# Performance work log

Hardware: AMD Instinct MI355X
Metric: run time of the kernel (lower is better)

The kernel has to match this reference:

```python
import jax, jax.numpy as jnp
import numpy as np

NEG = -1e30  # safe 'log zero' for fp32 (avoids -inf NaNs in grads)


def _ctc_loss(logits, targets, input_lengths, target_lengths):
    """PyTorch-semantics CTC loss: blank=0, reduction='mean', zero_infinity=True.
    logits: [B,T,C] (pre-log-softmax), targets: [B,S] padded, lengths: [B].
    """
    B, T, C = logits.shape
    S = targets.shape[1]
    L = 2 * S + 1  # extended target length (blanks interleaved)
    logp = jax.nn.log_softmax(logits, axis=-1)  # [B,T,C]

    # extended targets: blank, y1, blank, y2, ..., blank
    ext = jnp.zeros((B, L), jnp.int32).at[:, 1::2].set(targets.astype(jnp.int32))
    lp_ext = jnp.take_along_axis(
        logp, jnp.broadcast_to(ext[:, None, :], (B, T, L)), axis=2)  # [B,T,L]

    pos = jnp.arange(L)
    ext_m2 = jnp.pad(ext, ((0, 0), (2, 0)))[:, :L]
    can_skip = (ext != 0) & (ext != ext_m2) & (pos >= 2)  # [B,L]

    def shift(a, k):
        return jnp.pad(a, ((0, 0), (k, 0)), constant_values=NEG)[:, :L]

    def lse3(a, b, c):
        m = jnp.maximum(jnp.maximum(a, b), c)
        return m + jnp.log(jnp.exp(a - m) + jnp.exp(b - m) + jnp.exp(c - m))

    alpha0 = (jnp.full((B, L), NEG, logits.dtype)
              .at[:, 0].set(lp_ext[:, 0, 0])
              .at[:, 1].set(lp_ext[:, 0, 1]))

    def step(alpha, xs):
        lp_t, t = xs  # lp_t: [B,L]
        a2 = shift(alpha, 1)
        a3 = jnp.where(can_skip, shift(alpha, 2), NEG)
        new = lp_t + lse3(alpha, a2, a3)
        # freeze alpha once past each sample's input_length
        alpha = jnp.where((t < input_lengths)[:, None], new, alpha)
        return alpha, None

    lp_T = jnp.swapaxes(lp_ext, 0, 1)  # [T,B,L]
    alpha, _ = jax.lax.scan(step, alpha0, (lp_T[1:], jnp.arange(1, T)))

    i1 = (2 * target_lengths - 1).astype(jnp.int32)
    i2 = (2 * target_lengths).astype(jnp.int32)
    a_last = jnp.take_along_axis(alpha, i1[:, None], axis=1)[:, 0]
    a_blank = jnp.take_along_axis(alpha, i2[:, None], axis=1)[:, 0]
    loss = -jnp.logaddexp(a_last, a_blank)  # [B]
    loss = jnp.where(loss > 1e29, 0.0, loss)  # zero_infinity=True
    return jnp.mean(loss / target_lengths.astype(loss.dtype))


def setup_inputs() -> dict:
    key = jax.random.key(0)
    ks = jax.random.split(key, 8)
    B, T = 32, 2000
    C_err, S_err = 4, 50
    C_ph, S_ph = 64, 200
    error_logits = jax.random.normal(ks[0], (B, T, C_err), jnp.float32)
    phoneme_logits = jax.random.normal(ks[1], (B, T, C_ph), jnp.float32)
    # labels in [1, C): blank=0 never appears in targets
    error_targets = jax.random.randint(ks[2], (B, S_err), 1, C_err, jnp.int32)
    phoneme_targets = jax.random.randint(ks[3], (B, S_ph), 1, C_ph, jnp.int32)
    error_input_lengths = jax.random.randint(ks[4], (B,), T - T // 4, T + 1, jnp.int32)
    phoneme_input_lengths = jax.random.randint(ks[5], (B,), T - T // 4, T + 1, jnp.int32)
    error_target_lengths = jax.random.randint(ks[6], (B,), S_err // 2, S_err + 1, jnp.int32)
    phoneme_target_lengths = jax.random.randint(ks[7], (B,), S_ph // 2, S_ph + 1, jnp.int32)
    return {
        "error_logits": error_logits,
        "phoneme_logits": phoneme_logits,
        "error_targets": error_targets,
        "phoneme_targets": phoneme_targets,
        "error_input_lengths": error_input_lengths,
        "phoneme_input_lengths": phoneme_input_lengths,
        "error_target_lengths": error_target_lengths,
        "phoneme_target_lengths": phoneme_target_lengths,
    }


def reference(error_logits, phoneme_logits, error_targets, phoneme_targets,
              error_input_lengths, phoneme_input_lengths,
              error_target_lengths, phoneme_target_lengths):
    error_weight = 1.0
    phoneme_weight = 1.0
    error_loss = _ctc_loss(error_logits, error_targets,
                           error_input_lengths, error_target_lengths)
    phoneme_loss = _ctc_loss(phoneme_logits, phoneme_targets,
                             phoneme_input_lengths, phoneme_target_lengths)
    total_loss = error_weight * error_loss + phoneme_weight * phoneme_loss
    return total_loss
```

## Files before the change

kernel.cpp:

```cpp
#include <hip/hip_runtime.h>
#include <math.h>


static constexpr float  LOG2E = 1.4426950408889634f;
static constexpr double LN2D  = 0.6931471805599453;
static constexpr int GROWS = 2032;

#define DPP_WAVE_SHL1   0x130
#define DPP_WAVE_SHR1   0x138
#define DPP_ROW_SHR(n)  (0x110 | (n))
#define DPP_ROW_BCAST15 0x142
#define DPP_ROW_BCAST31 0x143

__device__ __forceinline__ float fexp2(float x) {
  return __builtin_amdgcn_exp2f(x);
}
__device__ __forceinline__ float flog2(float x) {
  return __builtin_amdgcn_logf(x);
}

__device__ __forceinline__ double dpp_shr1_f64(double x) {
  int lo = __double2loint(x), hi = __double2hiint(x);
  lo = __builtin_amdgcn_update_dpp(0, lo, DPP_WAVE_SHR1, 0xf, 0xf, true);
  hi = __builtin_amdgcn_update_dpp(0, hi, DPP_WAVE_SHR1, 0xf, 0xf, true);
  return __hiloint2double(hi, lo);
}

__device__ __forceinline__ double dpp_shl1_f64(double x) {
  int lo = __double2loint(x), hi = __double2hiint(x);
  lo = __builtin_amdgcn_update_dpp(0, lo, DPP_WAVE_SHL1, 0xf, 0xf, true);
  hi = __builtin_amdgcn_update_dpp(0, hi, DPP_WAVE_SHL1, 0xf, 0xf, true);
  return __hiloint2double(hi, lo);
}

__device__ __forceinline__ int imax2(int a, int b) { return a > b ? a : b; }

__device__ __forceinline__ int wave_imax(int v) {
  v = imax2(v, __builtin_amdgcn_update_dpp(0, v, DPP_ROW_SHR(1), 0xf, 0xf, true));
  v = imax2(v, __builtin_amdgcn_update_dpp(0, v, DPP_ROW_SHR(2), 0xf, 0xf, true));
  v = imax2(v, __builtin_amdgcn_update_dpp(0, v, DPP_ROW_SHR(4), 0xf, 0xf, true));
  v = imax2(v, __builtin_amdgcn_update_dpp(0, v, DPP_ROW_SHR(8), 0xf, 0xf, true));
  v = imax2(v, __builtin_amdgcn_update_dpp(0, v, DPP_ROW_BCAST15, 0xf, 0xf, true));
  v = imax2(v, __builtin_amdgcn_update_dpp(0, v, DPP_ROW_BCAST31, 0xf, 0xf, true));
  return __builtin_amdgcn_readlane(v, 63);
}


__global__ __launch_bounds__(256) void gather_ph_kernel(
    const float* __restrict__ ph_logits, const float* __restrict__ err_logits,
    const int* __restrict__ ph_tgt,
    float* __restrict__ Gph, float* __restrict__ Lpb_ph,
    float* __restrict__ Lpb_er, float* __restrict__ out) {
  const int bx = blockIdx.x, b = blockIdx.y;
  const int tid = threadIdx.x;
  const int lane = tid & 63, wv = tid >> 6;

  if (bx == 0 && b == 0 && tid == 0) *out = 0.f;

  if (wv == 0 && lane < 32) {
    const int t = bx * 32 + lane;
    if (t < 2000) {
      const float4 v = *(const float4*)(err_logits + ((size_t)b * 2000 + t) * 4);
      const float z0 = v.x * LOG2E;
      const float s = fexp2(z0) + fexp2(v.y * LOG2E) + fexp2(v.z * LOG2E) +
                      fexp2(v.w * LOG2E);
      Lpb_er[(size_t)b * GROWS + t] = z0 - flog2(s);
    }
  }

  const int* tb = ph_tgt + b * 200;
  int idx[4];
  float msk[4];
#pragma unroll
  for (int k = 0; k < 4; ++k) {
    const int si = lane * 4 + k;
    const int cls = (si < 200) ? tb[si] : 0;
    idx[k] = cls << 2;
    msk[k] = (si < 200) ? 1.0f : 0.0f;
  }
  const int t0 = (bx * 4 + wv) * 8;
  float z[8], e[8], s[8];
#pragma unroll
  for (int u = 0; u < 8; ++u) {
    const int t = t0 + u;
    const int tc = (t < 2000) ? t : 1999;
    z[u] = ph_logits[((size_t)b * 2000 + tc) * 64 + lane] * LOG2E;
    e[u] = fexp2(z[u]);
    s[u] = e[u];
  }
#pragma unroll
  for (int off = 32; off >= 1; off >>= 1) {
#pragma unroll
    for (int u = 0; u < 8; ++u) s[u] += __shfl_xor(s[u], off, 64);
  }
#pragma unroll
  for (int u = 0; u < 8; ++u) {
    const int t = t0 + u;
    if (t < 2000) {
      const float e0 = __int_as_float(
          __builtin_amdgcn_readlane(__float_as_int(e[u]), 0));
      const float inv0 = 1.0f / e0;
      float o[4];
#pragma unroll
      for (int k = 0; k < 4; ++k) {
        const float v = __int_as_float(
            __builtin_amdgcn_ds_bpermute(idx[k], __float_as_int(e[u])));
        o[k] = msk[k] * v * inv0;
      }
      *(float4*)(Gph + ((size_t)b * GROWS + t) * 256 + lane * 4) =
          make_float4(o[0], o[1], o[2], o[3]);
      if (lane == 0)
        Lpb_ph[(size_t)b * GROWS + t] = z[u] - flog2(s[u]);
    }
  }
}

template <int P> struct RowP { float v[P]; };

template <int P>
__device__ __forceinline__ void bl_renorm(double (&B)[P], double (&L)[P],
                                          int& K, int tgt) {
  double mm = B[0];
#pragma unroll
  for (int k = 0; k < P; ++k) mm = fmax(fmax(mm, B[k]), L[k]);
  const int ex = (__double2hiint(mm) >> 20) & 0x7ff;
  const int emax = wave_imax(ex);
  if (emax > 0) {
    int d = tgt - emax;
    if (d > 1023) d = 1023;
    if (d < -1022) d = -1022;
    const double sc = __hiloint2double((d + 1023) << 20, 0);
#pragma unroll
    for (int k = 0; k < P; ++k) { B[k] *= sc; L[k] *= sc; }
    K += d;
  }
}

template <int P>
__device__ __forceinline__ void bl_step(double (&B)[P], double (&L)[P],
                                        const double (&skipm)[P],
                                        const RowP<P>& f) {
  const double Lm1 = dpp_shr1_f64(L[P - 1]);
  double nB[P], nL[P];
#pragma unroll
  for (int k = 0; k < P; ++k) {
    const double Lp = (k >= 1) ? L[k - 1] : Lm1;
    nB[k] = B[k] + Lp;
    nL[k] = (double)f.v[k] * fma(skipm[k], Lp, B[k] + L[k]);
  }
#pragma unroll
  for (int k = 0; k < P; ++k) { B[k] = nB[k]; L[k] = nL[k]; }
}

template <int P>
__device__ __forceinline__ void bl_step_bwd(double (&B)[P], double (&L)[P],
                                            const double (&sknext)[P],
                                            const RowP<P>& f) {
  double w[P];
#pragma unroll
  for (int k = 0; k < P; ++k) w[k] = (double)f.v[k] * L[k];
  const double wN = dpp_shl1_f64(w[0]);
  const double BN = dpp_shl1_f64(B[0]);
  double nB[P], nL[P];
#pragma unroll
  for (int k = 0; k < P; ++k) {
    const double wp1 = (k < P - 1) ? w[k + 1] : wN;
    const double Bp1 = (k < P - 1) ? B[k + 1] : BN;
    nB[k] = B[k] + w[k];
    nL[k] = fma(sknext[k], wp1, w[k] + Bp1);
  }
#pragma unroll
  for (int k = 0; k < P; ++k) { B[k] = nB[k]; L[k] = nL[k]; }
}

__device__ __forceinline__ float spb_sum(const float* __restrict__ Lpb,
                                         int len, int lane) {
  float spb = 0.f;
  for (int t0 = lane; t0 < len; t0 += 512) {
#pragma unroll
    for (int u = 0; u < 8; ++u) {
      const int t = t0 + u * 64;
      const int tc = (t < len) ? t : 0;
      const float v = Lpb[tc];
      spb += (t < len) ? v : 0.0f;
    }
  }
#pragma unroll
  for (int off = 32; off >= 1; off >>= 1) spb += __shfl_xor(spb, off, 64);
  return spb;
}

template <int P, typename LdF, typename UseF>
__device__ __forceinline__ void run_fwd(int nsteps, LdF ldrow, UseF use,
                                        double (&B)[P], double (&L)[P],
                                        const double (&sk)[P], int& K) {
  using Buf = decltype(ldrow(1));
  const int ng = nsteps / 16;
  Buf bufA[16], bufB[16];
  if (ng >= 1) {
#pragma unroll
    for (int u = 0; u < 16; ++u) bufA[u] = ldrow(1 + u);
  }
  if (ng >= 2) {
#pragma unroll
    for (int u = 0; u < 16; ++u) bufB[u] = ldrow(17 + u);
  }
  int g = 0;
  for (; g + 2 <= ng; g += 2) {
    bl_renorm<P>(B, L, K, 1523);
    {
      const int gn = (g + 2 < ng) ? (g + 2) : 0;
#pragma unroll
      for (int u = 0; u < 16; ++u) {
        bl_step<P>(B, L, sk, use(bufA[u]));
        bufA[u] = ldrow(1 + gn * 16 + u);
      }
    }
    bl_renorm<P>(B, L, K, 1523);
    {
      const int gn = (g + 3 < ng) ? (g + 3) : 0;
#pragma unroll
      for (int u = 0; u < 16; ++u) {
        bl_step<P>(B, L, sk, use(bufB[u]));
        bufB[u] = ldrow(1 + gn * 16 + u);
      }
    }
  }
  if (g < ng) {
    bl_renorm<P>(B, L, K, 1523);
#pragma unroll
    for (int u = 0; u < 16; ++u) bl_step<P>(B, L, sk, use(bufA[u]));
    ++g;
  }
  {
    const int tstart = 1 + ng * 16;
    Buf bufT[15];
#pragma unroll
    for (int u = 0; u < 15; ++u) {
      int t = tstart + u;
      if (t > nsteps) t = (nsteps > 0) ? nsteps : 1;
      bufT[u] = ldrow(t);
    }
#pragma unroll
    for (int u = 0; u < 15; ++u) {
      if (tstart + u <= nsteps) {
        if (u == 0) bl_renorm<P>(B, L, K, 1523);
        bl_step<P>(B, L, sk, use(bufT[u]));
      }
    }
  }
}

template <int P, typename LdF, typename UseF>
__device__ __forceinline__ void run_bwd(int len, int M, LdF ldrow, UseF use,
                                        double (&B)[P], double (&L)[P],
                                        const double (&sk)[P], int& K) {
  using Buf = decltype(ldrow(1));
  const int ng = M / 16;
  Buf bufA[16], bufB[16];
  if (ng >= 1) {
#pragma unroll
    for (int u = 0; u < 16; ++u) bufA[u] = ldrow(len - 1 - u);
  }
  if (ng >= 2) {
#pragma unroll
    for (int u = 0; u < 16; ++u) bufB[u] = ldrow(len - 17 - u);
  }
  int g = 0;
  for (; g + 2 <= ng; g += 2) {
    bl_renorm<P>(B, L, K, 1023);
    {
      const int jb = (g + 2 < ng) ? (g + 2) * 16 : 0;
#pragma unroll
      for (int u = 0; u < 16; ++u) {
        bl_step_bwd<P>(B, L, sk, use(bufA[u]));
        bufA[u] = ldrow(len - 1 - jb - u);
      }
    }
    bl_renorm<P>(B, L, K, 1023);
    {
      const int jb = (g + 3 < ng) ? (g + 3) * 16 : 0;
#pragma unroll
      for (int u = 0; u < 16; ++u) {
        bl_step_bwd<P>(B, L, sk, use(bufB[u]));
        bufB[u] = ldrow(len - 1 - jb - u);
      }
    }
  }
  if (g < ng) {
    bl_renorm<P>(B, L, K, 1023);
#pragma unroll
    for (int u = 0; u < 16; ++u) bl_step_bwd<P>(B, L, sk, use(bufA[u]));
    ++g;
  }
  {
    const int jstart = ng * 16;
    Buf bufT[15];
#pragma unroll
    for (int u = 0; u < 15; ++u) {
      int j = jstart + u;
      if (j > M - 1) j = (M > 0) ? (M - 1) : 0;
      bufT[u] = ldrow(len - 1 - j);
    }
#pragma unroll
    for (int u = 0; u < 15; ++u) {
      if (jstart + u < M) {
        if (u == 0) bl_renorm<P>(B, L, K, 1023);
        bl_step_bwd<P>(B, L, sk, use(bufT[u]));
      }
    }
  }
}

__device__ __forceinline__ void chain_ph_fb(
    const float* __restrict__ Glab, const float* __restrict__ Lpb,
    const int* __restrict__ tb, int len, int tl, float* __restrict__ out,
    double* sBb, double* sLb, int* sKb) {
  constexpr int P = 4, S = 200, LSTRIDE = 256;
  const int tid = threadIdx.x;
  const int wave = tid >> 6, lane = tid & 63;
  const int t_mid = len >> 1;
  const int M = (len - 1) - t_mid;
  const float* gp = Glab + lane * P;

  auto ldrow = [&](int t) {
    RowP<P> r;
    const float4 a = *(const float4*)(gp + (size_t)t * LSTRIDE);
    r.v[0] = a.x; r.v[1] = a.y; r.v[2] = a.z; r.v[3] = a.w;
    return r;
  };
  auto use_id = [](const RowP<P>& r) { return r; };

  float spb = 0.f;
  double B[P], L[P];
  int Kf = 0;

  if (wave == 0) {
    spb = spb_sum(Lpb, len, lane);
    double skipm[P];
#pragma unroll
    for (int k = 0; k < P; ++k) {
      const int s = lane * P + k;
      skipm[k] = (s >= 1 && s < S && tb[s] != tb[s - 1]) ? 1.0 : 0.0;
    }
#pragma unroll
    for (int k = 0; k < P; ++k) { B[k] = 0.0; L[k] = 0.0; }
    {
      const float r0 = Glab[0];
      if (lane == 0) { B[0] = 1.0; L[0] = (double)r0; }
    }
    run_fwd<P>(t_mid, ldrow, use_id, B, L, skipm, Kf);
  } else {
    double sknext[P];
#pragma unroll
    for (int k = 0; k < P; ++k) {
      const int s = lane * P + k;
      sknext[k] = (s + 1 < S && tb[s + 1] != tb[s]) ? 1.0 : 0.0;
    }
    double Bb[P], Lb[P];
#pragma unroll
    for (int k = 0; k < P; ++k) {
      const int s = lane * P + k;
      Bb[k] = (s == tl) ? 1.0 : 0.0;
      Lb[k] = (s == tl - 1) ? 1.0 : 0.0;
    }
    int Kb = 0;
    run_bwd<P>(len, M, ldrow, use_id, Bb, Lb, sknext, Kb);
#pragma unroll
    for (int k = 0; k < P; ++k) {
      sBb[lane * P + k] = Bb[k];
      sLb[lane * P + k] = Lb[k];
    }
    if (lane == 0) *sKb = Kb;
  }
  __syncthreads();
  if (wave == 0) {
    double dot = 0.0;
#pragma unroll
    for (int k = 0; k < P; ++k)
      dot += B[k] * sBb[lane * P + k] + L[k] * sLb[lane * P + k];
#pragma unroll
    for (int off = 32; off >= 1; off >>= 1) dot += __shfl_xor(dot, off, 64);
    if (lane == 0) {
      const int K2 = Kf + *sKb;
      float loss = (float)((double)K2 * LN2D - log(dot) - (double)spb * LN2D);
      if (!(loss < 1e29f)) loss = 0.f;
      atomicAdd(out, loss / ((float)tl * 32.0f));
    }
  }
}

__device__ __forceinline__ void chain_er_fb(
    const float* __restrict__ zb, const float* __restrict__ Lpb,
    const int* __restrict__ tb, int len, int tl, float* __restrict__ out,
    double* sBb, double* sLb, int* sKb) {
  constexpr int P = 1, S = 50;
  const int tid = threadIdx.x;
  const int wave = tid >> 6, lane = tid & 63;
  const int t_mid = len >> 1;
  const int M = (len - 1) - t_mid;
  const float4* zr = (const float4*)zb;

  const int c1 = tb[(lane < S) ? lane : (S - 1)];
  const float fmask = (lane < S) ? 1.0f : 0.0f;

  auto ldrow = [&](int t) { return zr[t]; };
  auto mkf = [&](const float4& q) {
    RowP<P> f;
    const float zc = (c1 == 1) ? q.y : (c1 == 2) ? q.z : q.w;
    f.v[0] = fmask * fexp2((zc - q.x) * LOG2E);
    return f;
  };

  float spb = 0.f;
  double B[P], L[P];
  int Kf = 0;

  if (wave == 0) {
    spb = spb_sum(Lpb, len, lane);
    double skipm[P];
    skipm[0] =
        (lane >= 1 && lane < S && tb[lane] != tb[lane - 1]) ? 1.0 : 0.0;
    B[0] = 0.0; L[0] = 0.0;
    {
      const float4 q0 = zr[0];
      const int c0 = tb[0];
      const float zc = (c0 == 1) ? q0.y : (c0 == 2) ? q0.z : q0.w;
      if (lane == 0) {
        B[0] = 1.0;
        L[0] = (double)fexp2((zc - q0.x) * LOG2E);
      }
    }
    run_fwd<P>(t_mid, ldrow, mkf, B, L, skipm, Kf);
  } else {
    double sknext[P];
    sknext[0] = (lane + 1 < S && tb[lane + 1] != tb[lane]) ? 1.0 : 0.0;
    double Bb[P], Lb[P];
    Bb[0] = (lane == tl) ? 1.0 : 0.0;
    Lb[0] = (lane == tl - 1) ? 1.0 : 0.0;
    int Kb = 0;
    run_bwd<P>(len, M, ldrow, mkf, Bb, Lb, sknext, Kb);
    sBb[lane] = Bb[0];
    sLb[lane] = Lb[0];
    if (lane == 0) *sKb = Kb;
  }
  __syncthreads();
  if (wave == 0) {
    double dot = B[0] * sBb[lane] + L[0] * sLb[lane];
#pragma unroll
    for (int off = 32; off >= 1; off >>= 1) dot += __shfl_xor(dot, off, 64);
    if (lane == 0) {
      const int K2 = Kf + *sKb;
      float loss = (float)((double)K2 * LN2D - log(dot) - (double)spb * LN2D);
      if (!(loss < 1e29f)) loss = 0.f;
      atomicAdd(out, loss / ((float)tl * 32.0f));
    }
  }
}

__global__ __launch_bounds__(128) void ctc_chains_fbsplit_kernel(
    const float* __restrict__ Gph, const float* __restrict__ err_logits,
    const int* __restrict__ ph_tgt, const int* __restrict__ err_tgt,
    const int* __restrict__ err_il, const int* __restrict__ ph_il,
    const int* __restrict__ err_tl, const int* __restrict__ ph_tl,
    const float* __restrict__ Lpb_ph, const float* __restrict__ Lpb_er,
    float* __restrict__ out) {
  __shared__ double sBb[256], sLb[256];
  __shared__ int sKb;
  const int blk = blockIdx.x;
  if (blk < 32) {
    int len = err_il[blk]; if (len > 2000) len = 2000;
    chain_er_fb(err_logits + (size_t)blk * 2000 * 4,
                Lpb_er + (size_t)blk * GROWS, err_tgt + blk * 50, len,
                err_tl[blk], out, sBb, sLb, &sKb);
  } else {
    const int b = blk - 32;
    int len = ph_il[b]; if (len > 2000) len = 2000;
    chain_ph_fb(Gph + (size_t)b * GROWS * 256,
                Lpb_ph + (size_t)b * GROWS, ph_tgt + b * 200, len,
                ph_tl[b], out, sBb, sLb, &sKb);
  }
}


__global__ __launch_bounds__(256) void softmax4_kernel(
    const float* __restrict__ x, float* __restrict__ p, int nrows) {
  int r = blockIdx.x * blockDim.x + threadIdx.x;
  if (r >= nrows) return;
  float4 v = *reinterpret_cast<const float4*>(x + (size_t)r * 4);
  float z0 = v.x * LOG2E, z1 = v.y * LOG2E, z2 = v.z * LOG2E, z3 = v.w * LOG2E;
  float m = fmaxf(fmaxf(z0, z1), fmaxf(z2, z3));
  float e0 = fexp2(z0 - m), e1 = fexp2(z1 - m);
  float e2 = fexp2(z2 - m), e3 = fexp2(z3 - m);
  float inv = 1.0f / (e0 + e1 + e2 + e3);
  float4 o;
  o.x = e0 * inv; o.y = e1 * inv; o.z = e2 * inv; o.w = e3 * inv;
  *reinterpret_cast<float4*>(p + (size_t)r * 4) = o;
}

__global__ __launch_bounds__(256) void softmax64_kernel(
    const float* __restrict__ x, float* __restrict__ p, int nrows) {
  int row = blockIdx.x * 4 + (threadIdx.x >> 6);
  int lane = threadIdx.x & 63;
  if (row >= nrows) return;
  float z = x[(size_t)row * 64 + lane] * LOG2E;
  float m = z;
#pragma unroll
  for (int off = 32; off >= 1; off >>= 1) m = fmaxf(m, __shfl_xor(m, off, 64));
  float e = fexp2(z - m);
  float s = e;
#pragma unroll
  for (int off = 32; off >= 1; off >>= 1) s += __shfl_xor(s, off, 64);
  p[(size_t)row * 64 + lane] = e * (1.0f / s);
}

template <int C, int S, int R>
__device__ __forceinline__ void ctc_chain_lin_fb(
    const float* __restrict__ p_b, const int* __restrict__ tgt_b,
    int len, int tl, float* __restrict__ out, double* sa) {
  constexpr int L = 2 * S + 1;
  const int lane = threadIdx.x;
  int idx[R];
  double skipm[R];
#pragma unroll
  for (int j = 0; j < R; ++j) {
    const int l = lane * R + j;
    int cls = 0;
    bool sk = false;
    if (l & 1) {
      const int s = (l - 1) >> 1;
      const int sc = (s < S) ? s : (S - 1);
      cls = tgt_b[sc];
      if (s >= 1 && s < S) sk = (cls != tgt_b[s - 1]);
    }
    idx[j] = cls * 4;
    skipm[j] = sk ? 1.0 : 0.0;
  }
  double alpha[R];
#pragma unroll
  for (int j = 0; j < R; ++j) {
    const int l = lane * R + j;
    alpha[j] = (l <= 1) ? (double)p_b[idx[j] >> 2] : 0.0;
  }
  int K = 0;
  const int cl = lane & (C - 1);
  float rv = p_b[(size_t)((1 < len - 1) ? 1 : (len - 1)) * C + cl];
  float pf[R];
#pragma unroll
  for (int j = 0; j < R; ++j)
    pf[j] = __int_as_float(__builtin_amdgcn_ds_bpermute(idx[j], __float_as_int(rv)));
  rv = p_b[(size_t)((2 < len - 1) ? 2 : (len - 1)) * C + cl];
  for (int t = 1; t < len; ++t) {
    if ((t & 31) == 0) {
      double m = alpha[0];
#pragma unroll
      for (int j = 1; j < R; ++j) m = fmax(m, alpha[j]);
#pragma unroll
      for (int off = 1; off < 64; off <<= 1) m = fmax(m, __shfl_xor(m, off, 64));
      const long long bits = __double_as_longlong(m);
      const int e = (int)((bits >> 52) & 0x7FF);
      if (e > 0) {
        const double sc = __longlong_as_double((long long)(2046 - e) << 52);
#pragma unroll
        for (int j = 0; j < R; ++j) alpha[j] *= sc;
        K += 1023 - e;
      }
    }
    const int tn = (t + 2 < len) ? (t + 2) : (len - 1);
    const float rvn = p_b[(size_t)tn * C + cl];
    float pfn[R];
#pragma unroll
    for (int j = 0; j < R; ++j)
      pfn[j] = __int_as_float(__builtin_amdgcn_ds_bpermute(idx[j], __float_as_int(rv)));
    double am1 = __shfl_up(alpha[R - 1], 1, 64);
    double am2 = __shfl_up(alpha[R - 2], 1, 64);
    if (lane == 0) { am1 = 0.0; am2 = 0.0; }
    double na[R];
#pragma unroll
    for (int j = 0; j < R; ++j) {
      const double a0 = alpha[j];
      const double a1 = (j >= 1) ? alpha[j - 1] : am1;
      const double a2 = (j >= 2) ? alpha[j - 2] : ((j == 1) ? am1 : am2);
      double s = a0 + a1;
      s = fma(skipm[j], a2, s);
      na[j] = (double)pf[j] * s;
    }
#pragma unroll
    for (int j = 0; j < R; ++j) alpha[j] = na[j];
#pragma unroll
    for (int j = 0; j < R; ++j) pf[j] = pfn[j];
    rv = rvn;
  }
#pragma unroll
  for (int j = 0; j < R; ++j) {
    const int l = lane * R + j;
    if (l < L) sa[l] = alpha[j];
  }
  __syncthreads();
  if (lane == 0) {
    const double a = sa[2 * tl - 1] + sa[2 * tl];
    float loss = (float)((double)K * LN2D - log(a));
    if (!(loss < 1e29f)) loss = 0.0f;
    atomicAdd(out, loss / ((float)tl * 32.0f));
  }
}

__global__ __launch_bounds__(64) void ctc_chains_fb_kernel(
    const float* __restrict__ p_err, const float* __restrict__ p_ph,
    const int* __restrict__ err_tgt, const int* __restrict__ ph_tgt,
    const int* __restrict__ err_il, const int* __restrict__ ph_il,
    const int* __restrict__ err_tl, const int* __restrict__ ph_tl,
    float* __restrict__ out) {
  __shared__ double sa[512];
  const int T = 2000;
  const int blk = blockIdx.x;
  if (blk < 32) {
    const int b = blk;
    int len = err_il[b]; if (len > T) len = T;
    ctc_chain_lin_fb<4, 50, 2>(p_err + (size_t)b * T * 4, err_tgt + b * 50, len,
                               err_tl[b], out, sa);
  } else {
    const int b = blk - 32;
    int len = ph_il[b]; if (len > T) len = T;
    ctc_chain_lin_fb<64, 200, 7>(p_ph + (size_t)b * T * 64, ph_tgt + b * 200,
                                 len, ph_tl[b], out, sa);
  }
}


extern "C" void kernel_launch(void* const* d_in, const int* in_sizes, int n_in,
                              void* d_out, int out_size, void* d_ws,
                              size_t ws_size, hipStream_t stream) {
  const float* err_logits = (const float*)d_in[0];
  const float* ph_logits  = (const float*)d_in[1];
  const int* err_tgt = (const int*)d_in[2];
  const int* ph_tgt  = (const int*)d_in[3];
  const int* err_il  = (const int*)d_in[4];
  const int* ph_il   = (const int*)d_in[5];
  const int* err_tl  = (const int*)d_in[6];
  const int* ph_tl   = (const int*)d_in[7];
  float* out = (float*)d_out;

  const size_t gph = (size_t)32 * GROWS * 256;
  const size_t lpb = (size_t)32 * GROWS;
  const size_t need = (gph + 2 * lpb) * sizeof(float);

  if (ws_size >= need) {
    float* Gph = (float*)d_ws;
    float* Lpb_ph = Gph + gph;
    float* Lpb_er = Lpb_ph + lpb;
    gather_ph_kernel<<<dim3(63, 32), 256, 0, stream>>>(
        ph_logits, err_logits, ph_tgt, Gph, Lpb_ph, Lpb_er, out);
    ctc_chains_fbsplit_kernel<<<64, 128, 0, stream>>>(
        Gph, err_logits, ph_tgt, err_tgt, err_il, ph_il, err_tl, ph_tl,
        Lpb_ph, Lpb_er, out);
  } else {
    (void)hipMemsetAsync(d_out, 0, sizeof(float), stream);
    const int B = 32, T = 2000;
    const int rows = B * T;
    float* p_err = (float*)d_ws;
    float* p_ph  = p_err + (size_t)rows * 4;
    softmax4_kernel<<<(rows + 255) / 256, 256, 0, stream>>>(err_logits, p_err, rows);
    softmax64_kernel<<<(rows + 3) / 4, 256, 0, stream>>>(ph_logits, p_ph, rows);
    ctc_chains_fb_kernel<<<64, 64, 0, stream>>>(p_err, p_ph, err_tgt, ph_tgt,
                                                err_il, ph_il, err_tl, ph_tl, out);
  }
}
```

Baseline: 204.2 us.

## Split forward and backward CTC halves into separate one-wave blocks with merge kernel

Instead of a 128-thread block per chain with wave 0 running the forward half and wave 1 the backward half, each direction now runs in its own 64-thread block (128 blocks total). The two halves write their states to global workspace, and a new merge kernel computes the dot product and loss. This spreads the two serial recurrences across separate CUs instead of sharing one CU's SIMD resources. In exchange it adds a kernel launch and a global-memory round trip for the intermediate states.

Result: no change. 202.2 us (-1.0%).

```diff
diff --git a/kernel.cpp b/kernel.cpp
--- a/kernel.cpp
+++ b/kernel.cpp
@@ -312,173 +312,161 @@
   }
 }
 
-__device__ __forceinline__ void chain_ph_fb(
-    const float* __restrict__ Glab, const float* __restrict__ Lpb,
-    const int* __restrict__ tb, int len, int tl, float* __restrict__ out,
-    double* sBb, double* sLb, int* sKb) {
-  constexpr int P = 4, S = 200, LSTRIDE = 256;
-  const int tid = threadIdx.x;
-  const int wave = tid >> 6, lane = tid & 63;
-  const int t_mid = len >> 1;
-  const int M = (len - 1) - t_mid;
-  const float* gp = Glab + lane * P;
-
-  auto ldrow = [&](int t) {
-    RowP<P> r;
-    const float4 a = *(const float4*)(gp + (size_t)t * LSTRIDE);
-    r.v[0] = a.x; r.v[1] = a.y; r.v[2] = a.z; r.v[3] = a.w;
-    return r;
-  };
-  auto use_id = [](const RowP<P>& r) { return r; };
-
-  float spb = 0.f;
-  double B[P], L[P];
-  int Kf = 0;
-
-  if (wave == 0) {
-    spb = spb_sum(Lpb, len, lane);
-    double skipm[P];
-#pragma unroll
-    for (int k = 0; k < P; ++k) {
-      const int s = lane * P + k;
-      skipm[k] = (s >= 1 && s < S && tb[s] != tb[s - 1]) ? 1.0 : 0.0;
-    }
-#pragma unroll
-    for (int k = 0; k < P; ++k) { B[k] = 0.0; L[k] = 0.0; }
-    {
-      const float r0 = Glab[0];
-      if (lane == 0) { B[0] = 1.0; L[0] = (double)r0; }
-    }
-    run_fwd<P>(t_mid, ldrow, use_id, B, L, skipm, Kf);
-  } else {
-    double sknext[P];
-#pragma unroll
-    for (int k = 0; k < P; ++k) {
-      const int s = lane * P + k;
-      sknext[k] = (s + 1 < S && tb[s + 1] != tb[s]) ? 1.0 : 0.0;
-    }
-    double Bb[P], Lb[P];
-#pragma unroll
-    for (int k = 0; k < P; ++k) {
-      const int s = lane * P + k;
-      Bb[k] = (s == tl) ? 1.0 : 0.0;
-      Lb[k] = (s == tl - 1) ? 1.0 : 0.0;
-    }
-    int Kb = 0;
-    run_bwd<P>(len, M, ldrow, use_id, Bb, Lb, sknext, Kb);
-#pragma unroll
-    for (int k = 0; k < P; ++k) {
-      sBb[lane * P + k] = Bb[k];
-      sLb[lane * P + k] = Lb[k];
-    }
-    if (lane == 0) *sKb = Kb;
-  }
-  __syncthreads();
-  if (wave == 0) {
-    double dot = 0.0;
-#pragma unroll
-    for (int k = 0; k < P; ++k)
-      dot += B[k] * sBb[lane * P + k] + L[k] * sLb[lane * P + k];
-#pragma unroll
-    for (int off = 32; off >= 1; off >>= 1) dot += __shfl_xor(dot, off, 64);
-    if (lane == 0) {
-      const int K2 = Kf + *sKb;
-      float loss = (float)((double)K2 * LN2D - log(dot) - (double)spb * LN2D);
-      if (!(loss < 1e29f)) loss = 0.f;
-      atomicAdd(out, loss / ((float)tl * 32.0f));
-    }
-  }
-}
-
-__device__ __forceinline__ void chain_er_fb(
-    const float* __restrict__ zb, const float* __restrict__ Lpb,
-    const int* __restrict__ tb, int len, int tl, float* __restrict__ out,
-    double* sBb, double* sLb, int* sKb) {
-  constexpr int P = 1, S = 50;
-  const int tid = threadIdx.x;
-  const int wave = tid >> 6, lane = tid & 63;
-  const int t_mid = len >> 1;
-  const int M = (len - 1) - t_mid;
-  const float4* zr = (const float4*)zb;
-
-  const int c1 = tb[(lane < S) ? lane : (S - 1)];
-  const float fmask = (lane < S) ? 1.0f : 0.0f;
-
-  auto ldrow = [&](int t) { return zr[t]; };
-  auto mkf = [&](const float4& q) {
-    RowP<P> f;
-    const float zc = (c1 == 1) ? q.y : (c1 == 2) ? q.z : q.w;
-    f.v[0] = fmask * fexp2((zc - q.x) * LOG2E);
-    return f;
-  };
-
-  float spb = 0.f;
-  double B[P], L[P];
-  int Kf = 0;
-
-  if (wave == 0) {
-    spb = spb_sum(Lpb, len, lane);
-    double skipm[P];
-    skipm[0] =
-        (lane >= 1 && lane < S && tb[lane] != tb[lane - 1]) ? 1.0 : 0.0;
-    B[0] = 0.0; L[0] = 0.0;
-    {
-      const float4 q0 = zr[0];
-      const int c0 = tb[0];
-      const float zc = (c0 == 1) ? q0.y : (c0 == 2) ? q0.z : q0.w;
-      if (lane == 0) {
-        B[0] = 1.0;
-        L[0] = (double)fexp2((zc - q0.x) * LOG2E);
-      }
-    }
-    run_fwd<P>(t_mid, ldrow, mkf, B, L, skipm, Kf);
-  } else {
-    double sknext[P];
-    sknext[0] = (lane + 1 < S && tb[lane + 1] != tb[lane]) ? 1.0 : 0.0;
-    double Bb[P], Lb[P];
-    Bb[0] = (lane == tl) ? 1.0 : 0.0;
-    Lb[0] = (lane == tl - 1) ? 1.0 : 0.0;
-    int Kb = 0;
-    run_bwd<P>(len, M, ldrow, mkf, Bb, Lb, sknext, Kb);
-    sBb[lane] = Bb[0];
-    sLb[lane] = Lb[0];
-    if (lane == 0) *sKb = Kb;
-  }
-  __syncthreads();
-  if (wave == 0) {
-    double dot = B[0] * sBb[lane] + L[0] * sLb[lane];
-#pragma unroll
-    for (int off = 32; off >= 1; off >>= 1) dot += __shfl_xor(dot, off, 64);
-    if (lane == 0) {
-      const int K2 = Kf + *sKb;
-      float loss = (float)((double)K2 * LN2D - log(dot) - (double)spb * LN2D);
-      if (!(loss < 1e29f)) loss = 0.f;
-      atomicAdd(out, loss / ((float)tl * 32.0f));
-    }
-  }
-}
-
-__global__ __launch_bounds__(128) void ctc_chains_fbsplit_kernel(
+__global__ __launch_bounds__(64) void ctc_half_kernel(
     const float* __restrict__ Gph, const float* __restrict__ err_logits,
     const int* __restrict__ ph_tgt, const int* __restrict__ err_tgt,
     const int* __restrict__ err_il, const int* __restrict__ ph_il,
     const int* __restrict__ err_tl, const int* __restrict__ ph_tl,
     const float* __restrict__ Lpb_ph, const float* __restrict__ Lpb_er,
-    float* __restrict__ out) {
-  __shared__ double sBb[256], sLb[256];
-  __shared__ int sKb;
+    double* __restrict__ st, int* __restrict__ Ks,
+    float* __restrict__ spbA) {
   const int blk = blockIdx.x;
-  if (blk < 32) {
-    int len = err_il[blk]; if (len > 2000) len = 2000;
-    chain_er_fb(err_logits + (size_t)blk * 2000 * 4,
-                Lpb_er + (size_t)blk * GROWS, err_tgt + blk * 50, len,
-                err_tl[blk], out, sBb, sLb, &sKb);
+  const int dir = blk >> 6;
+  const int c = blk & 63;
+  const int lane = threadIdx.x;
+
+  double* stB = st + ((size_t)c * 4 + (dir ? 2 : 0)) * 256;
+  double* stL = st + ((size_t)c * 4 + (dir ? 3 : 1)) * 256;
+
+  if (c < 32) {
+    constexpr int P = 1, S = 50;
+    const int* tb = err_tgt + c * 50;
+    int len = err_il[c]; if (len > 2000) len = 2000;
+    const int tl = err_tl[c];
+    const int t_mid = len >> 1;
+    const int M = (len - 1) - t_mid;
+    const float4* zr = (const float4*)(err_logits + (size_t)c * 2000 * 4);
+
+    const int c1 = tb[(lane < S) ? lane : (S - 1)];
+    const float fmask = (lane < S) ? 1.0f : 0.0f;
+    auto ldrow = [&](int t) { return zr[t]; };
+    auto mkf = [&](const float4& q) {
+      RowP<P> f;
+      const float zc = (c1 == 1) ? q.y : (c1 == 2) ? q.z : q.w;
+      f.v[0] = fmask * fexp2((zc - q.x) * LOG2E);
+      return f;
+    };
+
+    double B[P], L[P];
+    int K = 0;
+    if (dir == 0) {
+      const float spb = spb_sum(Lpb_er + (size_t)c * GROWS, len, lane);
+      double skipm[P];
+      skipm[0] =
+          (lane >= 1 && lane < S && tb[lane] != tb[lane - 1]) ? 1.0 : 0.0;
+      B[0] = 0.0; L[0] = 0.0;
+      {
+        const float4 q0 = zr[0];
+        const int c0 = tb[0];
+        const float zc = (c0 == 1) ? q0.y : (c0 == 2) ? q0.z : q0.w;
+        if (lane == 0) {
+          B[0] = 1.0;
+          L[0] = (double)fexp2((zc - q0.x) * LOG2E);
+        }
+      }
+      run_fwd<P>(t_mid, ldrow, mkf, B, L, skipm, K);
+      if (lane == 0) spbA[c] = spb;
+    } else {
+      double sknext[P];
+      sknext[0] = (lane + 1 < S && tb[lane + 1] != tb[lane]) ? 1.0 : 0.0;
+      B[0] = (lane == tl) ? 1.0 : 0.0;
+      L[0] = (lane == tl - 1) ? 1.0 : 0.0;
+      run_bwd<P>(len, M, ldrow, mkf, B, L, sknext, K);
+    }
+    stB[lane] = B[0];
+    stL[lane] = L[0];
+    if (lane == 0) Ks[dir * 64 + c] = K;
   } else {
-    const int b = blk - 32;
+    constexpr int P = 4, S = 200, LSTRIDE = 256;
+    const int b = c - 32;
+    const int* tb = ph_tgt + b * 200;
     int len = ph_il[b]; if (len > 2000) len = 2000;
-    chain_ph_fb(Gph + (size_t)b * GROWS * 256,
-                Lpb_ph + (size_t)b * GROWS, ph_tgt + b * 200, len,
-                ph_tl[b], out, sBb, sLb, &sKb);
+    const int tl = ph_tl[b];
+    const int t_mid = len >> 1;
+    const int M = (len - 1) - t_mid;
+    const float* Glab = Gph + (size_t)b * GROWS * 256;
+    const float* gp = Glab + lane * P;
+
+    auto ldrow = [&](int t) {
+      RowP<P> r;
+      const float4 a = *(const float4*)(gp + (size_t)t * LSTRIDE);
+      r.v[0] = a.x; r.v[1] = a.y; r.v[2] = a.z; r.v[3] = a.w;
+      return r;
+    };
+    auto use_id = [](const RowP<P>& r) { return r; };
+
+    double B[P], L[P];
+    int K = 0;
+    if (dir == 0) {
+      const float spb = spb_sum(Lpb_ph + (size_t)b * GROWS, len, lane);
+      double skipm[P];
+#pragma unroll
+      for (int k = 0; k < P; ++k) {
+        const int s = lane * P + k;
+        skipm[k] = (s >= 1 && s < S && tb[s] != tb[s - 1]) ? 1.0 : 0.0;
+      }
+#pragma unroll
+      for (int k = 0; k < P; ++k) { B[k] = 0.0; L[k] = 0.0; }
+      {
+        const float r0 = Glab[0];
+        if (lane == 0) { B[0] = 1.0; L[0] = (double)r0; }
+      }
+      run_fwd<P>(t_mid, ldrow, use_id, B, L, skipm, K);
+      if (lane == 0) spbA[c] = spb;
+    } else {
+      double sknext[P];
+#pragma unroll
+      for (int k = 0; k < P; ++k) {
+        const int s = lane * P + k;
+        sknext[k] = (s + 1 < S && tb[s + 1] != tb[s]) ? 1.0 : 0.0;
+      }
+#pragma unroll
+      for (int k = 0; k < P; ++k) {
+        const int s = lane * P + k;
+        B[k] = (s == tl) ? 1.0 : 0.0;
+        L[k] = (s == tl - 1) ? 1.0 : 0.0;
+      }
+      run_bwd<P>(len, M, ldrow, use_id, B, L, sknext, K);
+    }
+#pragma unroll
+    for (int k = 0; k < P; ++k) {
+      stB[lane * P + k] = B[k];
+      stL[lane * P + k] = L[k];
+    }
+    if (lane == 0) Ks[dir * 64 + c] = K;
+  }
+}
+
+__global__ __launch_bounds__(64) void ctc_merge_kernel(
+    const double* __restrict__ st, const int* __restrict__ Ks,
+    const float* __restrict__ spbA, const int* __restrict__ err_tl,
+    const int* __restrict__ ph_tl, float* __restrict__ out) {
+  const int c = blockIdx.x;
+  const int lane = threadIdx.x;
+  const double* Bf = st + ((size_t)c * 4 + 0) * 256;
+  const double* Lf = st + ((size_t)c * 4 + 1) * 256;
+  const double* Bb = st + ((size_t)c * 4 + 2) * 256;
+  const double* Lb = st + ((size_t)c * 4 + 3) * 256;
+  double dot;
+  if (c < 32) {
+    dot = Bf[lane] * Bb[lane] + Lf[lane] * Lb[lane];
+  } else {
+    dot = 0.0;
+#pragma unroll
+    for (int k = 0; k < 4; ++k) {
+      const int i = lane * 4 + k;
+      dot += Bf[i] * Bb[i] + Lf[i] * Lb[i];
+    }
+  }
+#pragma unroll
+  for (int off = 32; off >= 1; off >>= 1) dot += __shfl_xor(dot, off, 64);
+  if (lane == 0) {
+    const int K2 = Ks[c] + Ks[64 + c];
+    const int tl = (c < 32) ? err_tl[c] : ph_tl[c - 32];
+    float loss =
+        (float)((double)K2 * LN2D - log(dot) - (double)spbA[c] * LN2D);
+    if (!(loss < 1e29f)) loss = 0.f;
+    atomicAdd(out, loss / ((float)tl * 32.0f));
   }
 }
 
@@ -643,17 +631,23 @@
 
   const size_t gph = (size_t)32 * GROWS * 256;
   const size_t lpb = (size_t)32 * GROWS;
-  const size_t need = (gph + 2 * lpb) * sizeof(float);
+  const size_t nst = (size_t)64 * 4 * 256;
+  const size_t need =
+      (gph + 2 * lpb) * sizeof(float) + nst * sizeof(double) + 256 * 4;
 
   if (ws_size >= need) {
     float* Gph = (float*)d_ws;
     float* Lpb_ph = Gph + gph;
     float* Lpb_er = Lpb_ph + lpb;
+    double* st = (double*)(Lpb_er + lpb);
+    int* Ks = (int*)(st + nst);
+    float* spbA = (float*)(Ks + 128);
     gather_ph_kernel<<<dim3(63, 32), 256, 0, stream>>>(
         ph_logits, err_logits, ph_tgt, Gph, Lpb_ph, Lpb_er, out);
-    ctc_chains_fbsplit_kernel<<<64, 128, 0, stream>>>(
+    ctc_half_kernel<<<128, 64, 0, stream>>>(
         Gph, err_logits, ph_tgt, err_tgt, err_il, ph_il, err_tl, ph_tl,
-        Lpb_ph, Lpb_er, out);
+        Lpb_ph, Lpb_er, st, Ks, spbA);
+    ctc_merge_kernel<<<64, 64, 0, stream>>>(st, Ks, spbA, err_tl, ph_tl, out);
   } else {
     (void)hipMemsetAsync(d_out, 0, sizeof(float), stream);
     const int B = 32, T = 2000;
```
